# Performance work log

Hardware: AMD Instinct MI355X
Metric: run time of the kernel (lower is better)

The kernel has to match this reference:

```python
import jax, jax.numpy as jnp
import numpy as np
import math

B, S, D, H, F, E, K, L, V = 1, 2048, 768, 12, 1536, 8, 2, 2, 32000


def _ln(x, w, b, eps=1e-5):
    m = x.mean(-1, keepdims=True)
    v = ((x - m) ** 2).mean(-1, keepdims=True)
    return (x - m) / jnp.sqrt(v + eps) * w + b


def setup_inputs() -> dict:
    key = jax.random.key(0)
    ks = jax.random.split(key, 16)
    std = 0.02
    inp = {
        'tokens': jax.random.randint(ks[0], (B, S), 0, V),
        'emb': jax.random.normal(ks[1], (V, D), jnp.float32) * std,
        'qkv_w': jax.random.normal(ks[2], (L, 3 * D, D), jnp.float32) * std,
        'qkv_b': jax.random.normal(ks[3], (L, 3 * D), jnp.float32) * std,
        'out_w': jax.random.normal(ks[4], (L, D, D), jnp.float32) * std,
        'out_b': jax.random.normal(ks[5], (L, D), jnp.float32) * std,
        'ln1_w': jnp.ones((L, D), jnp.float32),
        'ln1_b': jax.random.normal(ks[6], (L, D), jnp.float32) * std,
        'ln2_w': jnp.ones((L, D), jnp.float32),
        'ln2_b': jax.random.normal(ks[7], (L, D), jnp.float32) * std,
        'gate_w': jax.random.normal(ks[8], (L, E, D), jnp.float32) * std,
        'eg_w': jax.random.normal(ks[9], (L, E, F, D), jnp.float32) * std,
        'eu_w': jax.random.normal(ks[10], (L, E, F, D), jnp.float32) * std,
        'ed_w': jax.random.normal(ks[11], (L, E, D, F), jnp.float32) * std,
        'rms_w': jnp.ones((D,), jnp.float32),
    }
    return inp


def reference(tokens, emb, qkv_w, qkv_b, out_w, out_b, ln1_w, ln1_b,
              ln2_w, ln2_b, gate_w, eg_w, eu_w, ed_w, rms_w):
    Dh = D // H
    x = emb[tokens] * math.sqrt(D)  # (B,S,D)
    for l in range(L):
        # --- MultiheadAttention (batch_first, no mask, eval) ---
        qkv = x @ qkv_w[l].T + qkv_b[l]
        q, k, v = jnp.split(qkv, 3, axis=-1)
        q = q.reshape(B, S, H, Dh).transpose(0, 2, 1, 3)
        k = k.reshape(B, S, H, Dh).transpose(0, 2, 1, 3)
        v = v.reshape(B, S, H, Dh).transpose(0, 2, 1, 3)
        att = jax.nn.softmax(jnp.einsum('bhqd,bhkd->bhqk', q, k) / math.sqrt(Dh), axis=-1)
        o = jnp.einsum('bhqk,bhkd->bhqd', att, v).transpose(0, 2, 1, 3).reshape(B, S, D)
        o = o @ out_w[l].T + out_b[l]
        x = _ln(x + o, ln1_w[l], ln1_b[l])
        # --- SimpleDeepseekV3MoE: top-k gate, softmax over top-k scores ---
        gs = jnp.einsum('bsd,ed->bse', x, gate_w[l])
        topv, topi = jax.lax.top_k(gs, K)
        tw = jax.nn.softmax(topv, axis=-1)  # (B,S,K)
        # dense per-expert combine weight (0 for unselected experts)
        ew = jnp.sum(jax.nn.one_hot(topi, E, dtype=x.dtype) * tw[..., None], axis=-2)  # (B,S,E)
        hg = jax.nn.silu(jnp.einsum('bsd,efd->bsef', x, eg_w[l]))
        hu = jnp.einsum('bsd,efd->bsef', x, eu_w[l])
        ye = jnp.einsum('bsef,edf->bsed', hg * hu, ed_w[l])
        moe = jnp.einsum('bsed,bse->bsd', ye, ew)
        x = _ln(x + moe, ln2_w[l], ln2_b[l])
    # final RMSNorm (torch default eps=None -> finfo eps)
    rms = jnp.sqrt(jnp.mean(x * x, axis=-1, keepdims=True) + jnp.finfo(x.dtype).eps)
    x = x / rms * rms_w
    logits = x @ emb.T  # tied lm_head
    return logits
```

## Files before the change

### kernel.cpp

```cpp
#include <hip/hip_runtime.h>

#define SQ   2048
#define DM   768
#define NHD  12
#define DHD  64
#define FF   1536
#define NE   8
#define NL   2
#define NV   32000

typedef __attribute__((ext_vector_type(8))) short bf16x8;
typedef __attribute__((ext_vector_type(4))) float f32x4;

__device__ __forceinline__ unsigned short f2bf(float f) {
  unsigned u = __float_as_uint(f);
  return (unsigned short)((u + 0x7fffu + ((u >> 16) & 1u)) >> 16);
}
__device__ __forceinline__ float bf2f(unsigned short h) {
  return __uint_as_float(((unsigned)h) << 16);
}

#define GLD16(ldsp, gp) __builtin_amdgcn_global_load_lds( \
    (const __attribute__((address_space(1))) void*)(gp),  \
    (__attribute__((address_space(3))) void*)(ldsp), 16, 0, 0)

__device__ __forceinline__ void conv8(const float* s, unsigned short* d) {
  float4 a = *(const float4*)s;
  float4 b = *(const float4*)(s + 4);
  int4 pk = make_int4(
      (int)((unsigned)f2bf(a.x) | ((unsigned)f2bf(a.y) << 16)),
      (int)((unsigned)f2bf(a.z) | ((unsigned)f2bf(a.w) << 16)),
      (int)((unsigned)f2bf(b.x) | ((unsigned)f2bf(b.y) << 16)),
      (int)((unsigned)f2bf(b.z) | ((unsigned)f2bf(b.w) << 16)));
  *(int4*)d = pk;
}

__global__ __launch_bounds__(256) void conv_k(const float* __restrict__ s,
    unsigned short* __restrict__ d) {
  size_t i = (size_t)(blockIdx.x * 256 + threadIdx.x) * 8;
  conv8(s + i, d + i);
}

__global__ __launch_bounds__(256) void conv3_k(const float* __restrict__ s0,
    const float* __restrict__ s1, const float* __restrict__ s2,
    unsigned short* __restrict__ d, int per) {
  int b = blockIdx.x;
  const float* s = (b < per) ? s0 : (b < 2 * per) ? s1 : s2;
  int sb = (b < per) ? b : (b < 2 * per) ? b - per : b - 2 * per;
  size_t di = (size_t)b * 2048 + threadIdx.x * 8;
  size_t si = (size_t)sb * 2048 + threadIdx.x * 8;
  conv8(s + si, d + di);
}

__global__ __launch_bounds__(256) void conv2_k(const float* __restrict__ s0,
    const float* __restrict__ s1, unsigned short* __restrict__ d, int per0) {
  int b = blockIdx.x;
  const float* s = (b < per0) ? s0 : s1;
  int sb = (b < per0) ? b : b - per0;
  size_t di = (size_t)b * 2048 + threadIdx.x * 8;
  size_t si = (size_t)sb * 2048 + threadIdx.x * 8;
  conv8(s + si, d + di);
}

__global__ __launch_bounds__(256) void embed_k(const int* __restrict__ tok,
    const float* __restrict__ emb, float* __restrict__ x,
    unsigned short* __restrict__ xbf) {
  int idx = blockIdx.x * 256 + threadIdx.x;
  int s = idx / DM, d = idx % DM;
  float v = emb[(size_t)tok[s] * DM + d] * 27.712812921102035f;
  x[idx] = v;
  xbf[idx] = f2bf(v);
}

template<bool GATHER, bool OBF16>
__global__ __launch_bounds__(512) void gemm256_k(
    const unsigned short* __restrict__ A, long long lda,
    const unsigned short* __restrict__ B, long long ldb, long long b_z,
    void* __restrict__ C, long long ldc, long long c_z,
    int M, int Kd, int mT, int nT, int Z, int zmod,
    const int* __restrict__ glist, long long gl_z,
    const int* __restrict__ cnt)
{
  int nwg = gridDim.x, bid = blockIdx.x;
  int q = nwg >> 3, r = nwg & 7;
  int xcd = bid & 7, j = bid >> 3;
  int wid = (xcd < r ? xcd * (q + 1) : r * (q + 1) + (xcd - r) * q) + j;
  int z = wid % Z; int rem = wid / Z;
  int mt = rem % mT, nt = rem / mT;
  int zz = z % zmod;
  int Mz = cnt ? cnt[zz] : M;
  int m0 = mt * 128, n0 = nt * 256;
  if (m0 >= Mz) return;
  (void)nT;

  const unsigned short* Bz = B + (size_t)z * b_z;

  __shared__ __align__(16) unsigned short lds[3 * 6 * 4096];

  int t = threadIdx.x, w = t >> 6, lane = t & 63;
  int wm = (w >> 2) * 64, wn = (w & 3) * 64;
  int fr = lane & 15, ksg = lane >> 4;
  int lrow = lane >> 3;
  int lchunk = ((lane & 7) ^ lrow) * 8;

  const unsigned short* sp[6];
  #pragma unroll
  for (int hh = 0; hh < 2; ++hh) {
    int gr = m0 + hh * 64 + w * 8 + lrow; if (gr >= Mz) gr = Mz - 1;
    int arow;
    if constexpr (GATHER) arow = glist[(size_t)zz * gl_z + gr]; else arow = gr;
    sp[hh] = A + (size_t)arow * lda + lchunk;
  }
  #pragma unroll
  for (int hh = 0; hh < 4; ++hh)
    sp[2 + hh] = Bz + (size_t)(n0 + hh * 64 + w * 8 + lrow) * ldb + lchunk;

  int rdA = (w >> 2) * 4096;
  int rdB = (2 + (w & 3)) * 4096;
  int stDst = w * 512;

  int rx = fr & 7;
  int off0 = (ksg ^ rx) * 8;
  int off1 = ((4 + ksg) ^ rx) * 8;

  int KT = Kd >> 6;
  f32x4 acc[4][4] = {};

  #pragma unroll
  for (int h = 0; h < 6; ++h)
    GLD16(&lds[h * 4096 + stDst], sp[h]);
  #pragma unroll
  for (int h = 0; h < 6; ++h)
    GLD16(&lds[(6 + h) * 4096 + stDst], sp[h] + 64);
  asm volatile("s_waitcnt vmcnt(6)" ::: "memory");
  __builtin_amdgcn_s_barrier();
  __builtin_amdgcn_sched_barrier(0);

  int buf = 0;
  for (int kt = 0; kt < KT; ++kt) {
    const unsigned short* Abl = &lds[buf * 6 * 4096 + rdA];
    const unsigned short* Bbl = &lds[buf * 6 * 4096 + rdB];
    int pf = (kt + 2 < KT);
    int pbuf = buf + 2; if (pbuf >= 3) pbuf -= 3;
    unsigned short* pd = &lds[pbuf * 6 * 4096 + stDst];
    long long koff = (long long)(kt + 2) * 64;

    if (pf) {
      GLD16(pd + 0 * 4096, sp[0] + koff);
      GLD16(pd + 1 * 4096, sp[1] + koff);
      GLD16(pd + 2 * 4096, sp[2] + koff);
    }
    {
      bf16x8 af[4], bv[4];
      #pragma unroll
      for (int m = 0; m < 4; ++m)
        af[m] = *(const bf16x8*)&Abl[(m * 16 + fr) * 64 + off0];
      #pragma unroll
      for (int n = 0; n < 4; ++n)
        bv[n] = *(const bf16x8*)&Bbl[(n * 16 + fr) * 64 + off0];
      __builtin_amdgcn_s_setprio(1);
      #pragma unroll
      for (int m = 0; m < 4; ++m)
        #pragma unroll
        for (int n = 0; n < 4; ++n)
          acc[m][n] = __builtin_amdgcn_mfma_f32_16x16x32_bf16(
              af[m], bv[n], acc[m][n], 0, 0, 0);
      __builtin_amdgcn_s_setprio(0);
    }
    if (pf) {
      GLD16(pd + 3 * 4096, sp[3] + koff);
      GLD16(pd + 4 * 4096, sp[4] + koff);
      GLD16(pd + 5 * 4096, sp[5] + koff);
    }
    {
      bf16x8 af[4], bv[4];
      #pragma unroll
      for (int m = 0; m < 4; ++m)
        af[m] = *(const bf16x8*)&Abl[(m * 16 + fr) * 64 + off1];
      #pragma unroll
      for (int n = 0; n < 4; ++n)
        bv[n] = *(const bf16x8*)&Bbl[(n * 16 + fr) * 64 + off1];
      __builtin_amdgcn_s_setprio(1);
      #pragma unroll
      for (int m = 0; m < 4; ++m)
        #pragma unroll
        for (int n = 0; n < 4; ++n)
          acc[m][n] = __builtin_amdgcn_mfma_f32_16x16x32_bf16(
              af[m], bv[n], acc[m][n], 0, 0, 0);
      __builtin_amdgcn_s_setprio(0);
    }
    if (pf) {
      asm volatile("s_waitcnt vmcnt(6)" ::: "memory");
    } else if (kt + 1 < KT) {
      asm volatile("s_waitcnt vmcnt(0)" ::: "memory");
    }
    __builtin_amdgcn_s_barrier();
    __builtin_amdgcn_sched_barrier(0);
    buf = buf + 1; if (buf == 3) buf = 0;
  }

  int rb = ksg * 4;
  #pragma unroll
  for (int m = 0; m < 4; ++m) {
    #pragma unroll
    for (int n = 0; n < 4; ++n) {
      #pragma unroll
      for (int rr = 0; rr < 4; ++rr) {
        int row = m0 + wm + m * 16 + rb + rr;
        if (row >= Mz) continue;
        size_t off = (size_t)z * c_z + (size_t)row * ldc +
                     (n0 + wn + n * 16 + fr);
        if constexpr (OBF16) ((unsigned short*)C)[off] = f2bf(acc[m][n][rr]);
        else                 ((float*)C)[off] = acc[m][n][rr];
      }
    }
  }
}

template<bool GATHER, bool BIAS, bool OBF16>
__global__ __launch_bounds__(256) void gemm_k(
    const unsigned short* __restrict__ A, long long lda, long long a_z,
    const unsigned short* __restrict__ B, long long ldb, long long b_z,
    const float* __restrict__ bias,
    void* __restrict__ C, long long ldc, long long c_z,
    int M, int N, int Kd, float scale,
    const int* __restrict__ glist, long long gl_z,
    const int* __restrict__ cnt, int mT, int nT, int Z)
{
  int nwg = gridDim.x, bid = blockIdx.x;
  int q = nwg >> 3, r = nwg & 7;
  int xcd = bid & 7, j = bid >> 3;
  int wid = (xcd < r ? xcd * (q + 1) : r * (q + 1) + (xcd - r) * q) + j;
  int z = wid % Z; int rem = wid / Z;
  int mt = rem % mT, nt = rem / mT;

  int Mz = cnt ? cnt[z] : M;
  int m0 = mt * 128, n0 = nt * 128;
  if (m0 >= Mz) return;

  const unsigned short* Ab = A + (size_t)z * a_z;
  const unsigned short* Bb = B + (size_t)z * b_z;

  __shared__ __align__(16) unsigned short As[128 * 64];
  __shared__ __align__(16) unsigned short Bs[128 * 64];

  int t = threadIdx.x, w = t >> 6, lane = t & 63;
  int wm = (w >> 1) * 64, wn = (w & 1) * 64;
  int fr = lane & 15, ksg = lane >> 4;
  int lrow = lane >> 3;
  int lchunk = ((lane & 7) ^ lrow) * 8;

  const unsigned short* ap[4];
  const unsigned short* bp[4];
  unsigned short* la[4];
  unsigned short* lb[4];
  #pragma unroll
  for (int i = 0; i < 4; ++i) {
    int rrow = w * 32 + i * 8 + lrow;
    int gr = m0 + rrow; if (gr >= Mz) gr = Mz - 1;
    int arow; if constexpr (GATHER) arow = glist[(size_t)z * gl_z + gr]; else arow = gr;
    ap[i] = Ab + (size_t)arow * lda + lchunk;
    int br = n0 + rrow; if (br >= N) br = N - 1;
    bp[i] = Bb + (size_t)br * ldb + lchunk;
    la[i] = &As[(w * 32 + i * 8) * 64];
    lb[i] = &Bs[(w * 32 + i * 8) * 64];
  }

  int rx = fr & 7;
  int off0 = ((0 + ksg) ^ rx) * 8;
  int off1 = ((4 + ksg) ^ rx) * 8;

  f32x4 acc[4][4] = {};

  for (int k0 = 0; k0 < Kd; k0 += 64) {
    #pragma unroll
    for (int i = 0; i < 4; ++i) GLD16(la[i], ap[i] + k0);
    #pragma unroll
    for (int i = 0; i < 4; ++i) GLD16(lb[i], bp[i] + k0);
    __syncthreads();
    #pragma unroll
    for (int kb = 0; kb < 2; ++kb) {
      int offk = kb ? off1 : off0;
      bf16x8 af[4], bv[4];
      #pragma unroll
      for (int m = 0; m < 4; ++m)
        af[m] = *(const bf16x8*)&As[(wm + m * 16 + fr) * 64 + offk];
      #pragma unroll
      for (int n = 0; n < 4; ++n)
        bv[n] = *(const bf16x8*)&Bs[(wn + n * 16 + fr) * 64 + offk];
      #pragma unroll
      for (int m = 0; m < 4; ++m)
        #pragma unroll
        for (int n = 0; n < 4; ++n)
          acc[m][n] = __builtin_amdgcn_mfma_f32_16x16x32_bf16(
              af[m], bv[n], acc[m][n], 0, 0, 0);
    }
    __syncthreads();
  }

  int rb = ksg * 4;
  #pragma unroll
  for (int m = 0; m < 4; ++m) {
    #pragma unroll
    for (int n = 0; n < 4; ++n) {
      int col = n0 + wn + n * 16 + fr;
      if (col >= N) continue;
      #pragma unroll
      for (int rr = 0; rr < 4; ++rr) {
        int row = m0 + wm + m * 16 + rb + rr;
        if (row >= Mz) continue;
        float v = acc[m][n][rr] * scale;
        if constexpr (BIAS) v += bias[col];
        size_t off = (size_t)z * c_z + (size_t)row * ldc + col;
        if constexpr (OBF16) ((unsigned short*)C)[off] = f2bf(v);
        else                 ((float*)C)[off] = v;
      }
    }
  }
}

__global__ __launch_bounds__(256) void transpose_v_k(
    const unsigned short* __restrict__ qkv, unsigned short* __restrict__ vt) {
  int kt = blockIdx.x;
  int h  = blockIdx.y;
  __shared__ unsigned short tile[64][72];
  int t = threadIdx.x;
  int r = t >> 2;
  int c0 = (t & 3) * 16;
  const unsigned short* src =
      qkv + (size_t)(kt * 64 + r) * (3 * DM) + 2 * DM + h * DHD + c0;
  *(int4*)&tile[r][c0]     = *(const int4*)(src);
  *(int4*)&tile[r][c0 + 8] = *(const int4*)(src + 8);
  __syncthreads();
  unsigned u[8];
  #pragma unroll
  for (int j = 0; j < 8; ++j)
    u[j] = (unsigned)tile[c0 + 2 * j][r] | ((unsigned)tile[c0 + 2 * j + 1][r] << 16);
  unsigned short* dst = vt + (size_t)(h * DHD + r) * SQ + kt * 64 + c0;
  *(int4*)dst       = make_int4((int)u[0], (int)u[1], (int)u[2], (int)u[3]);
  *(int4*)(dst + 8) = make_int4((int)u[4], (int)u[5], (int)u[6], (int)u[7]);
}

__global__ __launch_bounds__(128) void flash_k(
    const unsigned short* __restrict__ qkv,
    const unsigned short* __restrict__ vt,
    unsigned short* __restrict__ o)
{
  int nwg = gridDim.x, bid = blockIdx.x;
  int cpx = nwg >> 3;
  int wid = (bid & 7) * cpx + (bid >> 3);
  int h  = wid >> 6;
  int qt = wid & 63;
  int q0 = qt * 32;

  __shared__ __align__(16) unsigned short Ks[128 * 64];
  __shared__ __align__(16) unsigned short Vs[128 * 64];
  __shared__ __align__(16) unsigned short Ps[2][16 * 136];

  int t = threadIdx.x, w = t >> 6, lane = t & 63;
  int fr = lane & 15, ksg = lane >> 4;
  int lrow = lane >> 3;
  int lchunk = ((lane & 7) ^ lrow) * 8;

  const unsigned short* qbase = qkv + (size_t)q0 * (3 * DM) + h * DHD;
  #pragma unroll
  for (int i = 0; i < 2; ++i) {
    int rrow = w * 16 + i * 8 + lrow;
    GLD16(&Ks[(w * 16 + i * 8) * 64], qbase + (size_t)rrow * (3 * DM) + lchunk);
  }
  __syncthreads();
  bf16x8 qf[2];
  {
    int row = w * 16 + fr, ph = fr & 7;
    qf[0] = *(const bf16x8*)&Ks[row * 64 + ((ksg ^ ph) * 8)];
    qf[1] = *(const bf16x8*)&Ks[row * 64 + (((4 + ksg) ^ ph) * 8)];
  }
  __syncthreads();

  const unsigned short* kbase = qkv + DM + h * DHD;
  const unsigned short* vb = vt + (size_t)(h * DHD) * SQ;

  f32x4 oacc[4] = {};
  float m_r[4] = {-1e30f, -1e30f, -1e30f, -1e30f};
  float l_r[4] = {0.f, 0.f, 0.f, 0.f};

  for (int kt = 0; kt < SQ / 128; ++kt) {
    int kk0 = kt * 128;
    #pragma unroll
    for (int i = 0; i < 8; ++i) {
      int rrow = w * 64 + i * 8 + lrow;
      GLD16(&Ks[(w * 64 + i * 8) * 64],
            kbase + (size_t)(kk0 + rrow) * (3 * DM) + lchunk);
    }
    #pragma unroll
    for (int i = 0; i < 8; ++i) {
      int p = w * 64 + i * 8 + lrow;
      GLD16(&Vs[(w * 64 + i * 8) * 64],
            vb + (size_t)(p >> 1) * SQ + kk0 + (p & 1) * 64 + lchunk);
    }
    __syncthreads();

    f32x4 sacc[8] = {};
    #pragma unroll
    for (int kb = 0; kb < 2; ++kb) {
      #pragma unroll
      for (int n = 0; n < 8; ++n) {
        int row = n * 16 + fr;
        bf16x8 bvv = *(const bf16x8*)&Ks[row * 64 +
            (((kb * 4 + ksg) ^ (fr & 7)) * 8)];
        sacc[n] = __builtin_amdgcn_mfma_f32_16x16x32_bf16(
            qf[kb], bvv, sacc[n], 0, 0, 0);
      }
    }

    #pragma unroll
    for (int r = 0; r < 4; ++r) {
      float mx = sacc[0][r];
      #pragma unroll
      for (int n = 1; n < 8; ++n) mx = fmaxf(mx, sacc[n][r]);
      mx = fmaxf(mx, __shfl_xor(mx, 1));
      mx = fmaxf(mx, __shfl_xor(mx, 2));
      mx = fmaxf(mx, __shfl_xor(mx, 4));
      mx = fmaxf(mx, __shfl_xor(mx, 8));
      float mn = fmaxf(m_r[r], mx * 0.125f);
      float resc = __expf(m_r[r] - mn);
      m_r[r] = mn;
      #pragma unroll
      for (int n = 0; n < 4; ++n) oacc[n][r] *= resc;
      float rs = 0.f;
      #pragma unroll
      for (int n = 0; n < 8; ++n) {
        float p = __expf(sacc[n][r] * 0.125f - mn);
        rs += p;
        Ps[w][(ksg * 4 + r) * 136 + n * 16 + fr] = f2bf(p);
      }
      rs += __shfl_xor(rs, 1);
      rs += __shfl_xor(rs, 2);
      rs += __shfl_xor(rs, 4);
      rs += __shfl_xor(rs, 8);
      l_r[r] = l_r[r] * resc + rs;
    }

    #pragma unroll
    for (int ksi = 0; ksi < 4; ++ksi) {
      bf16x8 pa = *(const bf16x8*)&Ps[w][fr * 136 + ksi * 32 + ksg * 8];
      #pragma unroll
      for (int n = 0; n < 4; ++n) {
        int p = (n * 16 + fr) * 2 + (ksi >> 1);
        int c = (ksi & 1) * 4 + ksg;
        bf16x8 bvv = *(const bf16x8*)&Vs[p * 64 + ((c ^ (p & 7)) * 8)];
        oacc[n] = __builtin_amdgcn_mfma_f32_16x16x32_bf16(
            pa, bvv, oacc[n], 0, 0, 0);
      }
    }
    __syncthreads();
  }

  unsigned short* ob = o + (size_t)(q0 + w * 16) * DM + h * DHD;
  #pragma unroll
  for (int r = 0; r < 4; ++r) {
    float invl = 1.f / l_r[r];
    int qrow = ksg * 4 + r;
    #pragma unroll
    for (int n = 0; n < 4; ++n)
      ob[(size_t)qrow * DM + n * 16 + fr] = f2bf(oacc[n][r] * invl);
  }
}

__global__ __launch_bounds__(256) void add_ln_k(const float* __restrict__ xin,
    const float* __restrict__ add, const float* __restrict__ w,
    const float* __restrict__ b, float* __restrict__ xout,
    unsigned short* __restrict__ xbf) {
  int row = blockIdx.x, t = threadIdx.x;
  const float* xi = xin + (size_t)row * DM;
  const float* ai = add + (size_t)row * DM;
  float v[3]; float s = 0.f, sq = 0.f;
  #pragma unroll
  for (int i = 0; i < 3; ++i) {
    int idx = t + i * 256;
    v[i] = xi[idx] + ai[idx];
    s += v[i]; sq += v[i] * v[i];
  }
  #pragma unroll
  for (int o = 32; o; o >>= 1) { s += __shfl_xor(s, o); sq += __shfl_xor(sq, o); }
  __shared__ float rsm[4], rqm[4];
  int wv = t >> 6;
  if ((t & 63) == 0) { rsm[wv] = s; rqm[wv] = sq; }
  __syncthreads();
  s = rsm[0] + rsm[1] + rsm[2] + rsm[3];
  sq = rqm[0] + rqm[1] + rqm[2] + rqm[3];
  float mean = s * (1.f / 768.f);
  float var = sq * (1.f / 768.f) - mean * mean;
  float inv = rsqrtf(var + 1e-5f);
  float* xo = xout + (size_t)row * DM;
  unsigned short* xb = xbf + (size_t)row * DM;
  #pragma unroll
  for (int i = 0; i < 3; ++i) {
    int idx = t + i * 256;
    float y = (v[i] - mean) * inv * w[idx] + b[idx];
    xo[idx] = y; xb[idx] = f2bf(y);
  }
}

__global__ void gate_topk_k(const float* __restrict__ x, const float* __restrict__ gw,
    float* __restrict__ tw, int* __restrict__ ti, int* __restrict__ cnt,
    int* __restrict__ lists, int* __restrict__ slot) {
  int sIdx = blockIdx.x, lane = threadIdx.x;
  const float* xr = x + (size_t)sIdx * DM;
  float acc[NE] = {};
  for (int d = lane; d < DM; d += 64) {
    float xv = xr[d];
    #pragma unroll
    for (int e = 0; e < NE; ++e) acc[e] += xv * gw[e * DM + d];
  }
  #pragma unroll
  for (int e = 0; e < NE; ++e) {
    #pragma unroll
    for (int o = 32; o; o >>= 1) acc[e] += __shfl_down(acc[e], o);
  }
  if (lane == 0) {
    float v0 = -1e30f, v1 = -1e30f; int i0 = 0, i1 = 0;
    #pragma unroll
    for (int e = 0; e < NE; ++e) {
      float v = acc[e];
      if (v > v0) { v1 = v0; i1 = i0; v0 = v; i0 = e; }
      else if (v > v1) { v1 = v; i1 = e; }
    }
    float e1 = expf(v1 - v0);
    float inv = 1.f / (1.f + e1);
    tw[sIdx * 2] = inv; tw[sIdx * 2 + 1] = e1 * inv;
    ti[sIdx * 2] = i0;  ti[sIdx * 2 + 1] = i1;
    int p0 = atomicAdd(&cnt[i0], 1); lists[i0 * SQ + p0] = sIdx; slot[sIdx * 2] = p0;
    int p1 = atomicAdd(&cnt[i1], 1); lists[i1 * SQ + p1] = sIdx; slot[sIdx * 2 + 1] = p1;
  }
}

__global__ void zero_k(int* __restrict__ c) {
  if (threadIdx.x < NE) c[threadIdx.x] = 0;
}

__global__ __launch_bounds__(256) void silu_mul_k(unsigned short* __restrict__ hg,
    const unsigned short* __restrict__ hu, const int* __restrict__ cnt) {
  int e = blockIdx.y, sl = blockIdx.x;
  if (sl >= cnt[e]) return;
  size_t base = ((size_t)e * SQ + sl) * FF;
  int t = threadIdx.x;
  #pragma unroll
  for (int i = 0; i < FF / 256; ++i) {
    size_t idx = base + t + i * 256;
    float g = bf2f(hg[idx]);
    float u = bf2f(hu[idx]);
    float sv = g / (1.f + expf(-g));
    hg[idx] = f2bf(sv * u);
  }
}

__global__ __launch_bounds__(256) void combine_ln_k(const float* __restrict__ xin,
    const float* __restrict__ ye, const float* __restrict__ tw,
    const int* __restrict__ ti, const int* __restrict__ slot,
    const float* __restrict__ w, const float* __restrict__ b,
    float* __restrict__ xout, unsigned short* __restrict__ xbf) {
  int row = blockIdx.x, t = threadIdx.x;
  int e0 = ti[row * 2], e1 = ti[row * 2 + 1];
  int p0 = slot[row * 2], p1 = slot[row * 2 + 1];
  float w0 = tw[row * 2], w1 = tw[row * 2 + 1];
  const float* y0 = ye + ((size_t)e0 * SQ + p0) * DM;
  const float* y1 = ye + ((size_t)e1 * SQ + p1) * DM;
  const float* xi = xin + (size_t)row * DM;
  float v[3]; float s = 0.f, sq = 0.f;
  #pragma unroll
  for (int i = 0; i < 3; ++i) {
    int idx = t + i * 256;
    v[i] = xi[idx] + w0 * y0[idx] + w1 * y1[idx];
    s += v[i]; sq += v[i] * v[i];
  }
  #pragma unroll
  for (int o = 32; o; o >>= 1) { s += __shfl_xor(s, o); sq += __shfl_xor(sq, o); }
  __shared__ float rsm[4], rqm[4];
  int wv = t >> 6;
  if ((t & 63) == 0) { rsm[wv] = s; rqm[wv] = sq; }
  __syncthreads();
  s = rsm[0] + rsm[1] + rsm[2] + rsm[3];
  sq = rqm[0] + rqm[1] + rqm[2] + rqm[3];
  float mean = s * (1.f / 768.f);
  float var = sq * (1.f / 768.f) - mean * mean;
  float inv = rsqrtf(var + 1e-5f);
  float* xo = xout + (size_t)row * DM;
  unsigned short* xb = xbf + (size_t)row * DM;
  #pragma unroll
  for (int i = 0; i < 3; ++i) {
    int idx = t + i * 256;
    float y = (v[i] - mean) * inv * w[idx] + b[idx];
    xo[idx] = y; xb[idx] = f2bf(y);
  }
}

__global__ __launch_bounds__(256) void rms_k(const float* __restrict__ x,
    const float* __restrict__ rw, unsigned short* __restrict__ xbf) {
  int row = blockIdx.x, t = threadIdx.x;
  const float* xi = x + (size_t)row * DM;
  float v[3]; float sq = 0.f;
  #pragma unroll
  for (int i = 0; i < 3; ++i) {
    int idx = t + i * 256;
    v[i] = xi[idx];
    sq += v[i] * v[i];
  }
  #pragma unroll
  for (int o = 32; o; o >>= 1) sq += __shfl_xor(sq, o);
  __shared__ float rqm[4];
  int wv = t >> 6;
  if ((t & 63) == 0) rqm[wv] = sq;
  __syncthreads();
  sq = rqm[0] + rqm[1] + rqm[2] + rqm[3];
  float inv = rsqrtf(sq * (1.f / 768.f) + 1.1920929e-07f);
  unsigned short* xb = xbf + (size_t)row * DM;
  #pragma unroll
  for (int i = 0; i < 3; ++i) {
    int idx = t + i * 256;
    xb[idx] = f2bf(v[i] * inv * rw[idx]);
  }
}

extern "C" void kernel_launch(void* const* d_in, const int* in_sizes, int n_in,
                              void* d_out, int out_size, void* d_ws, size_t ws_size,
                              hipStream_t stream) {
  (void)in_sizes; (void)n_in; (void)out_size; (void)ws_size;
  const int*   tokens = (const int*)d_in[0];
  const float* emb    = (const float*)d_in[1];
  const float* qkv_w  = (const float*)d_in[2];
  const float* qkv_b  = (const float*)d_in[3];
  const float* out_w  = (const float*)d_in[4];
  const float* out_b  = (const float*)d_in[5];
  const float* ln1_w  = (const float*)d_in[6];
  const float* ln1_b  = (const float*)d_in[7];
  const float* ln2_w  = (const float*)d_in[8];
  const float* ln2_b  = (const float*)d_in[9];
  const float* gate_w = (const float*)d_in[10];
  const float* eg_w   = (const float*)d_in[11];
  const float* eu_w   = (const float*)d_in[12];
  const float* ed_w   = (const float*)d_in[13];
  const float* rms_w  = (const float*)d_in[14];
  float* out = (float*)d_out;

  char* wsb = (char*)d_ws;
  float*          x_f    = (float*)(wsb + 0);
  unsigned short* x_bf   = (unsigned short*)(wsb + 6291456);
  unsigned short* qkv_bf = (unsigned short*)(wsb + 9437184);
  unsigned short* vt     = (unsigned short*)(wsb + 18874368);
  unsigned short* o_bf   = (unsigned short*)(wsb + 22020096);
  float*          tmp_f  = (float*)(wsb + 25165824);
  float*          tw     = (float*)(wsb + 31457280);
  int*            ti     = (int*)(wsb + 31473664);
  int*            cnt    = (int*)(wsb + 31490048);
  int*            lists  = (int*)(wsb + 31490304);
  int*            slot   = (int*)(wsb + 31555840);
  unsigned short* emb_bf = (unsigned short*)(wsb + 31572224);
  unsigned short* wbf    = (unsigned short*)(wsb + 80724224);
  unsigned short* hg     = (unsigned short*)(wsb + 142065920);
  unsigned short* hu     = (unsigned short*)(wsb + 142065920 + 50331648);
  float*          ye     = (float*)(wsb + 142065920 + 50331648);

  unsigned short* qw_bf = wbf;
  unsigned short* ow_bf = wbf + 1769472;
  unsigned short* eg_bf = wbf + 2359296;
  unsigned short* eu_bf = wbf + 11796480;
  unsigned short* ed_bf = wbf + 21233664;

  conv_k<<<12000, 256, 0, stream>>>(emb, emb_bf);
  embed_k<<<SQ * DM / 256, 256, 0, stream>>>(tokens, emb, x_f, x_bf);

  for (int l = 0; l < NL; ++l) {
    const float* qw = qkv_w + (size_t)l * 3 * DM * DM;
    const float* qb = qkv_b + (size_t)l * 3 * DM;
    const float* ob = out_b + (size_t)l * DM;
    const float* ow = out_w + (size_t)l * DM * DM;
    const float* gw = gate_w + (size_t)l * NE * DM;
    const float* egw = eg_w + (size_t)l * NE * FF * DM;
    const float* euw = eu_w + (size_t)l * NE * FF * DM;
    const float* edw = ed_w + (size_t)l * NE * DM * FF;

    conv2_k<<<1152, 256, 0, stream>>>(qw, ow, qw_bf, 864);
    conv3_k<<<13824, 256, 0, stream>>>(egw, euw, edw, eg_bf, 4608);

    gemm_k<false, true, true><<<16 * 18, 256, 0, stream>>>(
        x_bf, DM, 0, qw_bf, DM, 0, qb, qkv_bf, 3 * DM, 0,
        SQ, 3 * DM, DM, 1.f, nullptr, 0, nullptr, 16, 18, 1);

    transpose_v_k<<<dim3(SQ / 64, NHD), 256, 0, stream>>>(qkv_bf, vt);

    flash_k<<<NHD * 64, 128, 0, stream>>>(qkv_bf, vt, o_bf);

    gemm_k<false, true, false><<<16 * 6, 256, 0, stream>>>(
        o_bf, DM, 0, ow_bf, DM, 0, ob, tmp_f, DM, 0,
        SQ, DM, DM, 1.f, nullptr, 0, nullptr, 16, 6, 1);

    add_ln_k<<<SQ, 256, 0, stream>>>(x_f, tmp_f, ln1_w + l * DM, ln1_b + l * DM,
                                     x_f, x_bf);

    zero_k<<<1, 64, 0, stream>>>(cnt);
    gate_topk_k<<<SQ, 64, 0, stream>>>(x_f, gw, tw, ti, cnt, lists, slot);

    gemm256_k<true, true><<<16 * 6 * 16, 512, 0, stream>>>(
        x_bf, DM, eg_bf, DM, (long long)FF * DM,
        hg, FF, (long long)SQ * FF,
        SQ, DM, 16, 6, 16, 8, lists, SQ, cnt);

    silu_mul_k<<<dim3(SQ, NE), 256, 0, stream>>>(hg, hu, cnt);

    gemm_k<false, false, false><<<16 * 6 * NE, 256, 0, stream>>>(
        hg, FF, (long long)SQ * FF, ed_bf, FF, (long long)DM * FF, nullptr,
        ye, DM, (long long)SQ * DM,
        SQ, DM, FF, 1.f, nullptr, 0, cnt, 16, 6, NE);

    combine_ln_k<<<SQ, 256, 0, stream>>>(x_f, ye, tw, ti, slot,
                                         ln2_w + l * DM, ln2_b + l * DM,
                                         x_f, x_bf);
  }

  rms_k<<<SQ, 256, 0, stream>>>(x_f, rms_w, x_bf);

  gemm256_k<false, false><<<16 * 125, 512, 0, stream>>>(
      x_bf, DM, emb_bf, DM, 0, out, NV, 0,
      SQ, DM, 16, 125, 1, 1, nullptr, 0, nullptr);
}
```

Before: 813.1 us.

## Fuse V transpose into QKV GEMM, fuse LN1 with gate, new LM-head GEMM

The QKV GEMM epilogue now also writes the transposed V slice directly, which removes the separate transpose kernel. The post-attention add+LayerNorm is merged with the gate/top-k routing so the normalized row feeds the gate dot products without being re-read. The final logits GEMM switches from the 256-thread-tile kernel to a new 128x128, 256-thread, double-buffered kernel with 2 blocks/CU and interleaved prefetch. The V epilogue writes are strided, scattered 2-byte stores, and the gate step now adds an extra block-level sync.

Result: no change. 828.7 us (+1.9%).

```diff
diff --git a/kernel.cpp b/kernel.cpp
--- a/kernel.cpp
+++ b/kernel.cpp
@@ -70,6 +70,100 @@
   float v = emb[(size_t)tok[s] * DM + d] * 27.712812921102035f;
   x[idx] = v;
   xbf[idx] = f2bf(v);
+}
+
+__global__ __launch_bounds__(256, 2) void gemm8s_k(
+    const unsigned short* __restrict__ A, long long lda,
+    const unsigned short* __restrict__ B, long long ldb,
+    float* __restrict__ C, long long ldc,
+    int Kd, int mT)
+{
+  int nwg = gridDim.x, bid = blockIdx.x;
+  int q = nwg >> 3, r = nwg & 7;
+  int xcd = bid & 7, j = bid >> 3;
+  int wid = (xcd < r ? xcd * (q + 1) : r * (q + 1) + (xcd - r) * q) + j;
+  int mt = wid % mT, nt = wid / mT;
+  int m0 = mt * 128, n0 = nt * 128;
+
+  __shared__ __align__(16) unsigned short lds[2][2][8192];
+
+  int t = threadIdx.x, w = t >> 6, lane = t & 63;
+  int wm = w >> 1, wn = w & 1;
+  int fr = lane & 15, ksg = lane >> 4;
+  int lchunk = ((lane & 7) ^ (lane >> 3)) * 8;
+
+  const unsigned short* sa[4];
+  const unsigned short* sb[4];
+  #pragma unroll
+  for (int i = 0; i < 4; ++i) {
+    sa[i] = A + (size_t)(m0 + i * 32 + w * 8 + (lane >> 3)) * lda + lchunk;
+    sb[i] = B + (size_t)(n0 + i * 32 + w * 8 + (lane >> 3)) * ldb + lchunk;
+  }
+
+  int KT = Kd >> 6;
+  f32x4 acc[4][4] = {};
+
+#define STAGE_A8(bufi, k0) { _Pragma("unroll") \
+    for (int i = 0; i < 4; ++i) \
+      GLD16(&lds[bufi][0][(i * 32 + w * 8) * 64], sa[i] + (k0)); }
+#define STAGE_B8(bufi, k0) { _Pragma("unroll") \
+    for (int i = 0; i < 4; ++i) \
+      GLD16(&lds[bufi][1][(i * 32 + w * 8) * 64], sb[i] + (k0)); }
+
+  STAGE_A8(0, 0); STAGE_B8(0, 0);
+  asm volatile("s_waitcnt vmcnt(0)" ::: "memory");
+  __builtin_amdgcn_s_barrier();
+  __builtin_amdgcn_sched_barrier(0);
+
+  int buf = 0;
+  for (int kt = 0; kt < KT; ++kt) {
+    const unsigned short* Al = &lds[buf][0][0];
+    const unsigned short* Bl = &lds[buf][1][0];
+    int pf = (kt + 1 < KT);
+    long long koff = (long long)(kt + 1) * 64;
+    bf16x8 afr[4], bfr[4];
+    #pragma unroll
+    for (int ph = 0; ph < 2; ++ph) {
+      int ko = ((ph * 4 + ksg) ^ (fr & 7)) * 8;
+      #pragma unroll
+      for (int m = 0; m < 4; ++m)
+        afr[m] = *(const bf16x8*)&Al[(wm * 64 + m * 16 + fr) * 64 + ko];
+      #pragma unroll
+      for (int n = 0; n < 4; ++n)
+        bfr[n] = *(const bf16x8*)&Bl[(wn * 64 + n * 16 + fr) * 64 + ko];
+      if (pf) {
+        if (ph == 0) { STAGE_A8(buf ^ 1, koff); }
+        else         { STAGE_B8(buf ^ 1, koff); }
+      }
+      __builtin_amdgcn_s_barrier();
+      asm volatile("s_waitcnt lgkmcnt(0)" ::: "memory");
+      __builtin_amdgcn_sched_barrier(0);
+      __builtin_amdgcn_s_setprio(1);
+      #pragma unroll
+      for (int m = 0; m < 4; ++m)
+        #pragma unroll
+        for (int n = 0; n < 4; ++n)
+          acc[m][n] = __builtin_amdgcn_mfma_f32_16x16x32_bf16(
+              afr[m], bfr[n], acc[m][n], 0, 0, 0);
+      __builtin_amdgcn_s_setprio(0);
+      if (ph == 1 && pf) asm volatile("s_waitcnt vmcnt(0)" ::: "memory");
+      __builtin_amdgcn_s_barrier();
+      __builtin_amdgcn_sched_barrier(0);
+    }
+    buf ^= 1;
+  }
+#undef STAGE_A8
+#undef STAGE_B8
+
+  int rb = ksg * 4;
+  #pragma unroll
+  for (int m = 0; m < 4; ++m)
+    #pragma unroll
+    for (int n = 0; n < 4; ++n)
+      #pragma unroll
+      for (int rr = 0; rr < 4; ++rr)
+        C[(size_t)(m0 + wm * 64 + m * 16 + rb + rr) * ldc +
+          (n0 + wn * 64 + n * 16 + fr)] = acc[m][n][rr];
 }
 
 template<bool GATHER, bool OBF16>
@@ -217,7 +311,7 @@
   }
 }
 
-template<bool GATHER, bool BIAS, bool OBF16>
+template<bool GATHER, bool BIAS, bool OBF16, bool VT>
 __global__ __launch_bounds__(256) void gemm_k(
     const unsigned short* __restrict__ A, long long lda, long long a_z,
     const unsigned short* __restrict__ B, long long ldb, long long b_z,
@@ -225,7 +319,8 @@
     void* __restrict__ C, long long ldc, long long c_z,
     int M, int N, int Kd, float scale,
     const int* __restrict__ glist, long long gl_z,
-    const int* __restrict__ cnt, int mT, int nT, int Z)
+    const int* __restrict__ cnt, int mT, int nT, int Z,
+    unsigned short* __restrict__ vtout)
 {
   int nwg = gridDim.x, bid = blockIdx.x;
   int q = nwg >> 3, r = nwg & 7;
@@ -314,31 +409,13 @@
         size_t off = (size_t)z * c_z + (size_t)row * ldc + col;
         if constexpr (OBF16) ((unsigned short*)C)[off] = f2bf(v);
         else                 ((float*)C)[off] = v;
+        if constexpr (VT) {
+          if (n0 >= 2 * DM)
+            vtout[(size_t)(col - 2 * DM) * SQ + row] = f2bf(v);
+        }
       }
     }
   }
-}
-
-__global__ __launch_bounds__(256) void transpose_v_k(
-    const unsigned short* __restrict__ qkv, unsigned short* __restrict__ vt) {
-  int kt = blockIdx.x;
-  int h  = blockIdx.y;
-  __shared__ unsigned short tile[64][72];
-  int t = threadIdx.x;
-  int r = t >> 2;
-  int c0 = (t & 3) * 16;
-  const unsigned short* src =
-      qkv + (size_t)(kt * 64 + r) * (3 * DM) + 2 * DM + h * DHD + c0;
-  *(int4*)&tile[r][c0]     = *(const int4*)(src);
-  *(int4*)&tile[r][c0 + 8] = *(const int4*)(src + 8);
-  __syncthreads();
-  unsigned u[8];
-  #pragma unroll
-  for (int j = 0; j < 8; ++j)
-    u[j] = (unsigned)tile[c0 + 2 * j][r] | ((unsigned)tile[c0 + 2 * j + 1][r] << 16);
-  unsigned short* dst = vt + (size_t)(h * DHD + r) * SQ + kt * 64 + c0;
-  *(int4*)dst       = make_int4((int)u[0], (int)u[1], (int)u[2], (int)u[3]);
-  *(int4*)(dst + 8) = make_int4((int)u[4], (int)u[5], (int)u[6], (int)u[7]);
 }
 
 __global__ __launch_bounds__(128) void flash_k(
@@ -467,10 +544,12 @@
   }
 }
 
-__global__ __launch_bounds__(256) void add_ln_k(const float* __restrict__ xin,
+__global__ __launch_bounds__(256) void add_ln_gate_k(const float* __restrict__ xin,
     const float* __restrict__ add, const float* __restrict__ w,
-    const float* __restrict__ b, float* __restrict__ xout,
-    unsigned short* __restrict__ xbf) {
+    const float* __restrict__ b, const float* __restrict__ gw,
+    float* __restrict__ xout, unsigned short* __restrict__ xbf,
+    float* __restrict__ tw, int* __restrict__ ti, int* __restrict__ cnt,
+    int* __restrict__ lists, int* __restrict__ slot) {
   int row = blockIdx.x, t = threadIdx.x;
   const float* xi = xin + (size_t)row * DM;
   const float* ai = add + (size_t)row * DM;
@@ -484,8 +563,9 @@
   #pragma unroll
   for (int o = 32; o; o >>= 1) { s += __shfl_xor(s, o); sq += __shfl_xor(sq, o); }
   __shared__ float rsm[4], rqm[4];
-  int wv = t >> 6;
-  if ((t & 63) == 0) { rsm[wv] = s; rqm[wv] = sq; }
+  __shared__ float gsm[4][NE];
+  int wv = t >> 6, lane = t & 63;
+  if (lane == 0) { rsm[wv] = s; rqm[wv] = sq; }
   __syncthreads();
   s = rsm[0] + rsm[1] + rsm[2] + rsm[3];
   sq = rqm[0] + rqm[1] + rqm[2] + rqm[3];
@@ -494,44 +574,40 @@
   float inv = rsqrtf(var + 1e-5f);
   float* xo = xout + (size_t)row * DM;
   unsigned short* xb = xbf + (size_t)row * DM;
+  float y[3];
   #pragma unroll
   for (int i = 0; i < 3; ++i) {
     int idx = t + i * 256;
-    float y = (v[i] - mean) * inv * w[idx] + b[idx];
-    xo[idx] = y; xb[idx] = f2bf(y);
-  }
-}
-
-__global__ void gate_topk_k(const float* __restrict__ x, const float* __restrict__ gw,
-    float* __restrict__ tw, int* __restrict__ ti, int* __restrict__ cnt,
-    int* __restrict__ lists, int* __restrict__ slot) {
-  int sIdx = blockIdx.x, lane = threadIdx.x;
-  const float* xr = x + (size_t)sIdx * DM;
-  float acc[NE] = {};
-  for (int d = lane; d < DM; d += 64) {
-    float xv = xr[d];
-    #pragma unroll
-    for (int e = 0; e < NE; ++e) acc[e] += xv * gw[e * DM + d];
-  }
+    y[i] = (v[i] - mean) * inv * w[idx] + b[idx];
+    xo[idx] = y[i]; xb[idx] = f2bf(y[i]);
+  }
+  float p[NE];
   #pragma unroll
   for (int e = 0; e < NE; ++e) {
-    #pragma unroll
-    for (int o = 32; o; o >>= 1) acc[e] += __shfl_down(acc[e], o);
+    p[e] = y[0] * gw[e * DM + t] + y[1] * gw[e * DM + t + 256]
+         + y[2] * gw[e * DM + t + 512];
+    #pragma unroll
+    for (int o = 32; o; o >>= 1) p[e] += __shfl_xor(p[e], o);
   }
   if (lane == 0) {
+    #pragma unroll
+    for (int e = 0; e < NE; ++e) gsm[wv][e] = p[e];
+  }
+  __syncthreads();
+  if (t == 0) {
     float v0 = -1e30f, v1 = -1e30f; int i0 = 0, i1 = 0;
     #pragma unroll
     for (int e = 0; e < NE; ++e) {
-      float v = acc[e];
-      if (v > v0) { v1 = v0; i1 = i0; v0 = v; i0 = e; }
-      else if (v > v1) { v1 = v; i1 = e; }
+      float g = gsm[0][e] + gsm[1][e] + gsm[2][e] + gsm[3][e];
+      if (g > v0) { v1 = v0; i1 = i0; v0 = g; i0 = e; }
+      else if (g > v1) { v1 = g; i1 = e; }
     }
     float e1 = expf(v1 - v0);
-    float inv = 1.f / (1.f + e1);
-    tw[sIdx * 2] = inv; tw[sIdx * 2 + 1] = e1 * inv;
-    ti[sIdx * 2] = i0;  ti[sIdx * 2 + 1] = i1;
-    int p0 = atomicAdd(&cnt[i0], 1); lists[i0 * SQ + p0] = sIdx; slot[sIdx * 2] = p0;
-    int p1 = atomicAdd(&cnt[i1], 1); lists[i1 * SQ + p1] = sIdx; slot[sIdx * 2 + 1] = p1;
+    float invs = 1.f / (1.f + e1);
+    tw[row * 2] = invs; tw[row * 2 + 1] = e1 * invs;
+    ti[row * 2] = i0;   ti[row * 2 + 1] = i1;
+    int p0 = atomicAdd(&cnt[i0], 1); lists[i0 * SQ + p0] = row; slot[row * 2] = p0;
+    int p1 = atomicAdd(&cnt[i1], 1); lists[i1 * SQ + p1] = row; slot[row * 2 + 1] = p1;
   }
 }
 
@@ -664,7 +740,6 @@
   unsigned short* qw_bf = wbf;
   unsigned short* ow_bf = wbf + 1769472;
   unsigned short* eg_bf = wbf + 2359296;
-  unsigned short* eu_bf = wbf + 11796480;
   unsigned short* ed_bf = wbf + 21233664;
 
   conv_k<<<12000, 256, 0, stream>>>(emb, emb_bf);
@@ -683,23 +758,19 @@
     conv2_k<<<1152, 256, 0, stream>>>(qw, ow, qw_bf, 864);
     conv3_k<<<13824, 256, 0, stream>>>(egw, euw, edw, eg_bf, 4608);
 
-    gemm_k<false, true, true><<<16 * 18, 256, 0, stream>>>(
+    gemm_k<false, true, true, true><<<16 * 18, 256, 0, stream>>>(
         x_bf, DM, 0, qw_bf, DM, 0, qb, qkv_bf, 3 * DM, 0,
-        SQ, 3 * DM, DM, 1.f, nullptr, 0, nullptr, 16, 18, 1);
-
-    transpose_v_k<<<dim3(SQ / 64, NHD), 256, 0, stream>>>(qkv_bf, vt);
+        SQ, 3 * DM, DM, 1.f, nullptr, 0, nullptr, 16, 18, 1, vt);
 
     flash_k<<<NHD * 64, 128, 0, stream>>>(qkv_bf, vt, o_bf);
 
-    gemm_k<false, true, false><<<16 * 6, 256, 0, stream>>>(
+    gemm_k<false, true, false, false><<<16 * 6, 256, 0, stream>>>(
         o_bf, DM, 0, ow_bf, DM, 0, ob, tmp_f, DM, 0,
-        SQ, DM, DM, 1.f, nullptr, 0, nullptr, 16, 6, 1);
-
-    add_ln_k<<<SQ, 256, 0, stream>>>(x_f, tmp_f, ln1_w + l * DM, ln1_b + l * DM,
-                                     x_f, x_bf);
+        SQ, DM, DM, 1.f, nullptr, 0, nullptr, 16, 6, 1, nullptr);
 
     zero_k<<<1, 64, 0, stream>>>(cnt);
-    gate_topk_k<<<SQ, 64, 0, stream>>>(x_f, gw, tw, ti, cnt, lists, slot);
+    add_ln_gate_k<<<SQ, 256, 0, stream>>>(x_f, tmp_f, ln1_w + l * DM,
+        ln1_b + l * DM, gw, x_f, x_bf, tw, ti, cnt, lists, slot);
 
     gemm256_k<true, true><<<16 * 6 * 16, 512, 0, stream>>>(
         x_bf, DM, eg_bf, DM, (long long)FF * DM,
@@ -708,10 +779,10 @@
 
     silu_mul_k<<<dim3(SQ, NE), 256, 0, stream>>>(hg, hu, cnt);
 
-    gemm_k<false, false, false><<<16 * 6 * NE, 256, 0, stream>>>(
+    gemm_k<false, false, false, false><<<16 * 6 * NE, 256, 0, stream>>>(
         hg, FF, (long long)SQ * FF, ed_bf, FF, (long long)DM * FF, nullptr,
         ye, DM, (long long)SQ * DM,
-        SQ, DM, FF, 1.f, nullptr, 0, cnt, 16, 6, NE);
+        SQ, DM, FF, 1.f, nullptr, 0, cnt, 16, 6, NE, nullptr);
 
     combine_ln_k<<<SQ, 256, 0, stream>>>(x_f, ye, tw, ti, slot,
                                          ln2_w + l * DM, ln2_b + l * DM,
@@ -720,7 +791,6 @@
 
   rms_k<<<SQ, 256, 0, stream>>>(x_f, rms_w, x_bf);
 
-  gemm256_k<false, false><<<16 * 125, 512, 0, stream>>>(
-      x_bf, DM, emb_bf, DM, 0, out, NV, 0,
-      SQ, DM, 16, 125, 1, 1, nullptr, 0, nullptr);
-}
+  gemm8s_k<<<16 * 250, 256, 0, stream>>>(
+      x_bf, DM, emb_bf, DM, out, NV, DM, 16);
+}
```
